# Kernel tuning notes

Measured on AMD Instinct MI355X. Metric: run time of the kernel, lower is better.

The kernel has to match this reference:

```python
import jax, jax.numpy as jnp
import numpy as np

B, S, D = 2, 2048, 1024
H, DK = 16, 64            # n_heads, d_k = d_model // n_heads
EXP = 4                   # pattern-separation expand_factor
ED = DK * EXP             # expanded_dim = 256
TOPK = 32                 # top-k kept after ReLU expansion
ALPHA = 0.05
TNT = 1.0                 # trace_norm_target


def setup_inputs() -> dict:
    key = jax.random.key(0)
    ks = jax.random.split(key, 8)
    sc = 1.0 / np.sqrt(D)
    x = jax.random.normal(ks[0], (B, S, D), jnp.float32)
    W_q = jax.random.normal(ks[1], (D, D), jnp.float32) * sc
    W_k = jax.random.normal(ks[2], (D, D), jnp.float32) * sc
    W_v = jax.random.normal(ks[3], (D, D), jnp.float32) * sc
    W_o = jax.random.normal(ks[4], (D, D), jnp.float32) * sc
    # trace buffers (non-zero so the trace read path actually matters)
    traces = jax.random.normal(ks[5], (H, DK, DK), jnp.float32) * 0.02
    value_traces = jax.random.normal(ks[6], (H, ED, DK), jnp.float32) * 0.02
    # frozen random expansion projection (dentate gyrus), W / sqrt(d_k)
    W_expand = jax.random.normal(ks[7], (DK, ED), jnp.float32) / np.sqrt(DK)
    return dict(x=x, W_q=W_q, W_k=W_k, W_v=W_v, W_o=W_o,
                traces=traces, value_traces=value_traces, W_expand=W_expand)


def _eff_alpha(T):
    # alpha / (1 + ||T_h||_F / trace_norm_target), shape (1, H, 1, 1)
    norms = jnp.sqrt(jnp.sum(T * T, axis=(1, 2)))
    return (ALPHA / (1.0 + norms / TNT)).reshape(1, -1, 1, 1)


def _forward(x, W_q, W_k, W_v, W_o, traces, value_traces, W_expand):
    b, s, d = x.shape
    def proj(W):
        return jnp.einsum('bsd,de->bse', x, W).reshape(b, s, H, DK).transpose(0, 2, 1, 3)
    Q, K, V = proj(W_q), proj(W_k), proj(W_v)  # (B, H, S, DK)

    scores = jnp.einsum('bhqd,bhkd->bhqk', Q, K)
    # score trace bias: alpha_eff * (Q @ T @ K^T)
    QT = jnp.einsum('bhqd,hde->bhqe', Q, traces)
    trace_scores = jnp.einsum('bhqe,bhke->bhqk', QT, K)
    scores = (scores + _eff_alpha(traces) * trace_scores) / np.sqrt(DK)
    A = jax.nn.softmax(scores, axis=-1)
    out = jnp.einsum('bhqk,bhkd->bhqd', A, V)

    # value trace read with use_key_q shift: address with previous token's Q
    Q_addr = jnp.concatenate([jnp.zeros_like(Q[:, :, :1, :]), Q[:, :, :-1, :]], axis=2)
    # pattern separation: frozen random expansion + ReLU + top-k sparsify
    Q_exp = jax.nn.relu(jnp.einsum('bhsd,de->bhse', Q_addr, W_expand))  # (B,H,S,ED)
    kth = jax.lax.top_k(Q_exp, TOPK)[0][..., -1:]
    Q_sparse = jnp.where(Q_exp >= kth, Q_exp, 0.0)  # == scatter of top-k vals (ties at 0 contribute 0)
    stored = jnp.einsum('bhse,hed->bhsd', Q_sparse, value_traces)
    out = out + _eff_alpha(value_traces) * stored

    out = out.transpose(0, 2, 1, 3).reshape(b, s, d)
    return jnp.einsum('bsd,de->bse', out, W_o)


def reference(x, W_q, W_k, W_v, W_o, traces, value_traces, W_expand):
    return _forward(x, W_q, W_k, W_v, W_o, traces, value_traces, W_expand)
```

## Files before the change

kernel.cpp:

```cpp
#include <hip/hip_runtime.h>
#include <stdint.h>

#define Bn 2
#define Sn 2048
#define Dn 1024
#define Hn 16
#define DKn 64
#define EDn 256

typedef __attribute__((ext_vector_type(8))) short bvec8;
typedef __attribute__((ext_vector_type(4))) float fvec4;

#define MFMA(a, b, c) __builtin_amdgcn_mfma_f32_16x16x32_bf16(a, b, c, 0, 0, 0)

__device__ __forceinline__ float b2f(unsigned short u) {
  return __uint_as_float(((unsigned)u) << 16);
}
__device__ __forceinline__ unsigned short f2b(float x) {
  unsigned u = __float_as_uint(x);
  u += 0x7fffu + ((u >> 16) & 1u);
  return (unsigned short)(u >> 16);
}
__device__ __forceinline__ void g2l(const unsigned short* g, unsigned short* l) {
  __builtin_amdgcn_global_load_lds(
      (const __attribute__((address_space(1))) void*)g,
      (__attribute__((address_space(3))) void*)l, 16, 0, 0);
}
__device__ __forceinline__ int dpp_sum16(int x) {
  x += __builtin_amdgcn_update_dpp(0, x, 0x140, 0xf, 0xf, true);
  x += __builtin_amdgcn_update_dpp(0, x, 0x141, 0xf, 0xf, true);
  x += __builtin_amdgcn_update_dpp(0, x, 0x1B, 0xf, 0xf, true);
  x += __builtin_amdgcn_update_dpp(0, x, 0xB1, 0xf, 0xf, true);
  return x;
}
__device__ __forceinline__ unsigned dpp_umax16(unsigned x) {
  unsigned t;
  t = (unsigned)__builtin_amdgcn_update_dpp(0, (int)x, 0x140, 0xf, 0xf, true);
  x = x > t ? x : t;
  t = (unsigned)__builtin_amdgcn_update_dpp(0, (int)x, 0x141, 0xf, 0xf, true);
  x = x > t ? x : t;
  t = (unsigned)__builtin_amdgcn_update_dpp(0, (int)x, 0x1B, 0xf, 0xf, true);
  x = x > t ? x : t;
  t = (unsigned)__builtin_amdgcn_update_dpp(0, (int)x, 0xB1, 0xf, 0xf, true);
  x = x > t ? x : t;
  return x;
}

__global__ __launch_bounds__(256) void k_alphas(
    const float* __restrict__ traces, const float* __restrict__ vtr,
    float* __restrict__ alphas) {
  int blk = blockIdx.x;
  const float* base;
  int n;
  if (blk < 16) { base = traces + blk * DKn * DKn; n = DKn * DKn; }
  else          { base = vtr + (blk - 16) * EDn * DKn; n = EDn * DKn; }
  float s = 0.f;
  for (int i = threadIdx.x; i < n; i += 256) { float v = base[i]; s += v * v; }
  __shared__ float red[256];
  red[threadIdx.x] = s;
  __syncthreads();
  for (int off = 128; off > 0; off >>= 1) {
    if (threadIdx.x < off) red[threadIdx.x] += red[threadIdx.x + off];
    __syncthreads();
  }
  if (threadIdx.x == 0) alphas[blk] = 0.05f / (1.f + sqrtf(red[0]));
}

__global__ __launch_bounds__(256) void k_trW(
    const float* __restrict__ w0, const float* __restrict__ w1,
    const float* __restrict__ w2, const float* __restrict__ w3,
    unsigned short* __restrict__ dst) {
  int z = blockIdx.z;
  const float* src = (z == 0) ? w0 : ((z == 1) ? w1 : ((z == 2) ? w2 : w3));
  unsigned short* d = dst + (size_t)z * Dn * Dn;
  __shared__ unsigned short Tl[64][72];
  int tid = threadIdx.x;
  int k0 = blockIdx.y * 64, n0 = blockIdx.x * 64;
#pragma unroll
  for (int i = 0; i < 4; ++i) {
    int q = tid + 256 * i;
    int kr = q >> 4, c4 = q & 15;
    float4 v = *(const float4*)&src[(size_t)(k0 + kr) * Dn + n0 + 4 * c4];
    ushort4 u;
    u.x = f2b(v.x); u.y = f2b(v.y); u.z = f2b(v.z); u.w = f2b(v.w);
    *(ushort4*)&Tl[kr][4 * c4] = u;
  }
  __syncthreads();
#pragma unroll
  for (int i = 0; i < 4; ++i) {
    int q = tid + 256 * i;
    int nr = q >> 4, c4 = q & 15;
    ushort4 u;
    u.x = Tl[4 * c4 + 0][nr]; u.y = Tl[4 * c4 + 1][nr];
    u.z = Tl[4 * c4 + 2][nr]; u.w = Tl[4 * c4 + 3][nr];
    *(ushort4*)&d[(size_t)(n0 + nr) * Dn + k0 + 4 * c4] = u;
  }
}

__global__ __launch_bounds__(256) void k_mkM(const float* __restrict__ tr,
                                             const float* __restrict__ alph,
                                             unsigned short* __restrict__ Mt) {
  int h = blockIdx.x;
  float a = alph[h] * 0.125f;
  const float* th = tr + (size_t)h * DKn * DKn;
  unsigned short* mh = Mt + (size_t)h * DKn * DKn;
  for (int i = threadIdx.x; i < DKn * DKn; i += 256) {
    int e = i >> 6, k = i & 63;
    float v = a * th[(size_t)k * DKn + e] + ((e == k) ? 0.125f : 0.f);
    mh[i] = f2b(v);
  }
}

__global__ __launch_bounds__(256) void k_trVT2(const float* __restrict__ vtr,
                                               const float* __restrict__ Wexp,
                                               unsigned short* __restrict__ VTt,
                                               unsigned short* __restrict__ WexpT) {
  int e0 = blockIdx.x * 64;
  int h = blockIdx.y;
  __shared__ unsigned short Tl[64][72];
  int tid = threadIdx.x;
  if (h < 16) {
    const float* src = vtr + (size_t)h * EDn * DKn;
    unsigned short* dst = VTt + (size_t)h * DKn * EDn;
#pragma unroll
    for (int i = 0; i < 4; ++i) {
      int q = tid + 256 * i;
      int er = q >> 4, c4 = q & 15;
      float4 v = *(const float4*)&src[(size_t)(e0 + er) * DKn + 4 * c4];
      ushort4 u;
      u.x = f2b(v.x); u.y = f2b(v.y); u.z = f2b(v.z); u.w = f2b(v.w);
      *(ushort4*)&Tl[er][4 * c4] = u;
    }
    __syncthreads();
#pragma unroll
    for (int i = 0; i < 4; ++i) {
      int q = tid + 256 * i;
      int dr = q >> 4, c4 = q & 15;
      ushort4 u;
      u.x = Tl[4 * c4 + 0][dr]; u.y = Tl[4 * c4 + 1][dr];
      u.z = Tl[4 * c4 + 2][dr]; u.w = Tl[4 * c4 + 3][dr];
      *(ushort4*)&dst[(size_t)dr * EDn + e0 + 4 * c4] = u;
    }
  } else {
#pragma unroll
    for (int i = 0; i < 4; ++i) {
      int q = tid + 256 * i;
      int dr = q >> 4, c4 = q & 15;
      float4 v = *(const float4*)&Wexp[(size_t)dr * EDn + e0 + 4 * c4];
      ushort4 u;
      u.x = f2b(v.x); u.y = f2b(v.y); u.z = f2b(v.z); u.w = f2b(v.w);
      *(ushort4*)&Tl[dr][4 * c4] = u;
    }
    __syncthreads();
#pragma unroll
    for (int i = 0; i < 4; ++i) {
      int q = tid + 256 * i;
      int er = q >> 4, c4 = q & 15;
      ushort4 u;
      u.x = Tl[4 * c4 + 0][er]; u.y = Tl[4 * c4 + 1][er];
      u.z = Tl[4 * c4 + 2][er]; u.w = Tl[4 * c4 + 3][er];
      *(ushort4*)&WexpT[(size_t)(e0 + er) * DKn + 4 * c4] = u;
    }
  }
}

__global__ __launch_bounds__(256) void k_xb(const float* __restrict__ x,
                                            unsigned short* __restrict__ xb) {
  size_t i = ((size_t)blockIdx.x * 256 + threadIdx.x) * 4;
  float4 v = *(const float4*)&x[i];
  ushort4 u;
  u.x = f2b(v.x); u.y = f2b(v.y); u.z = f2b(v.z); u.w = f2b(v.w);
  *(ushort4*)&xb[i] = u;
}

template <int MODE>
__global__ __launch_bounds__(256) void k_gemm(
    const unsigned short* __restrict__ Ab, const float* __restrict__ Af,
    const unsigned short* __restrict__ BtBase, unsigned short* __restrict__ Qb,
    unsigned short* __restrict__ Kb, unsigned short* __restrict__ VtOut,
    float* __restrict__ Cout) {
  const int z = (MODE == 0) ? blockIdx.z : 0;
  const unsigned short* Bt = BtBase + (size_t)z * Dn * Dn;
  __shared__ unsigned short As[128 * 32];
  __shared__ unsigned short Bs[128 * 32];
  const int tid = threadIdx.x;
  const int w = tid >> 6, lane = tid & 63, qd = lane >> 4, cc = lane & 15;
  const int m0 = blockIdx.y * 128, n0 = blockIdx.x * 128;
  const int mW = 64 * (w >> 1), nW = 64 * (w & 1);
  const int srow = lane >> 2;
  const int schk = 8 * ((lane & 3) ^ (srow & 3));
  const int r0 = 32 * w + srow, r1 = r0 + 16;
  fvec4 acc[4][4];
#pragma unroll
  for (int i = 0; i < 4; ++i)
#pragma unroll
    for (int j = 0; j < 4; ++j) acc[i][j] = (fvec4){0.f, 0.f, 0.f, 0.f};

  for (int k0 = 0; k0 < Dn; k0 += 32) {
    if (MODE == 0) {
      g2l(&Ab[(size_t)(m0 + r0) * Dn + k0 + schk], &As[1024 * w]);
      g2l(&Ab[(size_t)(m0 + r1) * Dn + k0 + schk], &As[1024 * w + 512]);
    } else {
#pragma unroll
      for (int i = 0; i < 4; ++i) {
        int q = tid + 256 * i;
        int row = q >> 3, c4 = q & 7;
        float4 v = *(const float4*)&Af[(size_t)(m0 + row) * Dn + k0 + 4 * c4];
        ushort4 u;
        u.x = f2b(v.x); u.y = f2b(v.y); u.z = f2b(v.z); u.w = f2b(v.w);
        *(ushort4*)&As[row * 32 + 8 * ((c4 >> 1) ^ (row & 3)) + 4 * (c4 & 1)] =
            u;
      }
    }
    g2l(&Bt[(size_t)(n0 + r0) * Dn + k0 + schk], &Bs[1024 * w]);
    g2l(&Bt[(size_t)(n0 + r1) * Dn + k0 + schk], &Bs[1024 * w + 512]);
    __syncthreads();
    bvec8 af[4], bf[4];
#pragma unroll
    for (int i = 0; i < 4; ++i) {
      int ra = mW + 16 * i + cc;
      af[i] = *(const bvec8*)&As[ra * 32 + 8 * (qd ^ (ra & 3))];
      int rb = nW + 16 * i + cc;
      bf[i] = *(const bvec8*)&Bs[rb * 32 + 8 * (qd ^ (rb & 3))];
    }
#pragma unroll
    for (int i = 0; i < 4; ++i)
#pragma unroll
      for (int j = 0; j < 4; ++j) acc[i][j] = MFMA(af[i], bf[j], acc[i][j]);
    __syncthreads();
  }
#pragma unroll
  for (int i = 0; i < 4; ++i)
#pragma unroll
    for (int j = 0; j < 4; ++j) {
      int rowb = m0 + mW + 16 * i + 4 * qd;
      int col = n0 + nW + 16 * j + cc;
      if (MODE == 0) {
        int b = rowb >> 11, s = rowb & 2047;
        int h = col >> 6, dk = col & 63;
        if (z == 2) {
          ushort4 u;
          u.x = f2b(acc[i][j][0]); u.y = f2b(acc[i][j][1]);
          u.z = f2b(acc[i][j][2]); u.w = f2b(acc[i][j][3]);
          *(ushort4*)&VtOut[(((size_t)(b * Hn + h)) * DKn + dk) * Sn + s] = u;
        } else {
          unsigned short* Cb = (z == 0) ? Qb : Kb;
#pragma unroll
          for (int r = 0; r < 4; ++r)
            Cb[(((size_t)(b * Hn + h)) * Sn + s + r) * DKn + dk] =
                f2b(acc[i][j][r]);
        }
      } else {
#pragma unroll
        for (int r = 0; r < 4; ++r)
          Cout[(size_t)(rowb + r) * Dn + col] = acc[i][j][r];
      }
    }
}

__global__ __launch_bounds__(256, 4) void k_pattsep(
    const unsigned short* __restrict__ Qb,
    const unsigned short* __restrict__ WexpT,
    const unsigned short* __restrict__ VTt,
    const float* __restrict__ alphas, float* __restrict__ AT) {
  __shared__ uint4 Ps4[4][256];
  const int tile = blockIdx.x, bh = blockIdx.y;
  const int b = bh >> 4, h = bh & 15;
  const int tid = threadIdx.x;
  const int w = tid >> 6, lane = tid & 63, qd = lane >> 4, cc = lane & 15;
  const float avt = alphas[16 + h];

  const unsigned short* vtab = VTt + (size_t)h * DKn * EDn;
  unsigned short* Pw = (unsigned short*)Ps4[w];

  const int s0 = tile * 64 + w * 16;
  bvec8 aq0 = {}, aq1 = {};
  const int srow = s0 + cc;
  if (srow > 0) {
    const unsigned short* qp = Qb + ((size_t)bh * Sn + srow - 1) * DKn;
    aq0 = *(const bvec8*)&qp[8 * qd];
    aq1 = *(const bvec8*)&qp[32 + 8 * qd];
  }
  fvec4 E[16];
#pragma unroll
  for (int j = 0; j < 16; ++j) {
    const int e = 16 * j + cc;
    const unsigned short* wr = WexpT + (size_t)e * 64;
    bvec8 b0 = *(const bvec8*)&wr[8 * qd];
    bvec8 b1 = *(const bvec8*)&wr[32 + 8 * qd];
    fvec4 zv = {0.f, 0.f, 0.f, 0.f};
    zv = MFMA(aq0, b0, zv);
    E[j] = MFMA(aq1, b1, zv);
  }
#pragma unroll
  for (int j = 0; j < 16; ++j)
#pragma unroll
    for (int r = 0; r < 4; ++r) E[j][r] = fmaxf(E[j][r], 0.f);

  float thr[4];
#pragma unroll
  for (int r = 0; r < 4; ++r) {
    unsigned mx = 0u;
#pragma unroll
    for (int j = 0; j < 16; ++j) {
      unsigned e = __float_as_uint(E[j][r]);
      mx = mx > e ? mx : e;
    }
    mx = dpp_umax16(mx);
    {
      unsigned o = (unsigned)__shfl_xor((int)mx, 16);
      mx = mx > o ? mx : o;
      o = (unsigned)__shfl_xor((int)mx, 32);
      mx = mx > o ? mx : o;
    }
    int bstart = (mx == 0u) ? -1 : (31 - __clz((int)mx));
    bstart = __builtin_amdgcn_readfirstlane(bstart);
    unsigned cur = 0u;
    bool done = false;
    for (int bit = bstart; bit >= 0; --bit) {
      unsigned cand = cur | (1u << bit);
      float t = __uint_as_float(cand);
      int cnt = 0;
#pragma unroll
      for (int j = 0; j < 16; ++j) cnt += (E[j][r] >= t) ? 1 : 0;
      cnt = dpp_sum16(cnt);
      if (!done && cnt >= 32) {
        cur = cand;
        if (cnt == 32) done = true;
      }
      if (__all(done)) break;
    }
    thr[r] = __uint_as_float(cur);
  }

  fvec4 acc2[4];
#pragma unroll
  for (int j2 = 0; j2 < 4; ++j2) acc2[j2] = (fvec4){0.f, 0.f, 0.f, 0.f};

#pragma unroll
  for (int half = 0; half < 2; ++half) {
#pragma unroll
    for (int j = 0; j < 8; ++j) {
      const int jj = j + 8 * half;
#pragma unroll
      for (int r = 0; r < 4; ++r) {
        float v = E[jj][r];
        bool sel = (v >= thr[r]) && (v > 0.f);
        int row = 4 * qd + r;
        int s = 16 * j + cc;
        int ch = (s >> 3) ^ (row & 7);
        Pw[row * 128 + ch * 8 + (s & 7)] = sel ? f2b(v) : (unsigned short)0;
      }
    }
#pragma unroll
    for (int j2 = 0; j2 < 4; ++j2) {
      const int d = 16 * j2 + cc;
      const unsigned short* vr = vtab + (size_t)d * 256;
#pragma unroll
      for (int c = 0; c < 4; ++c) {
        int cg = 4 * (c + 4 * half) + qd;
        bvec8 bv = *(const bvec8*)&vr[8 * cg];
        int ca = 4 * c + qd;
        bvec8 ap = *(const bvec8*)&Pw[cc * 128 + 8 * (ca ^ (cc & 7))];
        acc2[j2] = MFMA(ap, bv, acc2[j2]);
      }
    }
  }
#pragma unroll
  for (int j2 = 0; j2 < 4; ++j2)
#pragma unroll
    for (int r = 0; r < 4; ++r) {
      int row = s0 + 4 * qd + r;
      AT[((size_t)(b * Sn + row)) * Dn + h * DKn + 16 * j2 + cc] =
          avt * acc2[j2][r];
    }
}

__global__ __launch_bounds__(256, 2) void k_attn(
    const unsigned short* __restrict__ Qb, const unsigned short* __restrict__ Kb,
    const unsigned short* __restrict__ Vt, const unsigned short* __restrict__ Mt,
    float* __restrict__ AT) {
  __shared__ unsigned short Kd[3][64 * 64];
  __shared__ unsigned short Vl[3][64 * 64];
  __shared__ unsigned short Ps[4][32 * 64];
  const int bh = blockIdx.x, qt = blockIdx.y;
  const int b = bh >> 4, h = bh & 15;
  const int tid = threadIdx.x;
  const int w = tid >> 6, lane = tid & 63, qd = lane >> 4, cc = lane & 15;
  const float L2E = 1.4426950408889634f;
  const float NB = 23.083120654223414f;

  const unsigned short* qg = Qb + ((size_t)bh * Sn + qt * 128 + w * 32) * DKn;
  const unsigned short* mh = Mt + (size_t)h * DKn * DKn;
  unsigned short* Pw = Ps[w];
  bvec8 mb0[4], mb1[4];
#pragma unroll
  for (int j = 0; j < 4; ++j) {
    mb0[j] = *(const bvec8*)&mh[(size_t)(16 * j + cc) * DKn + 8 * qd];
    mb1[j] = *(const bvec8*)&mh[(size_t)(16 * j + cc) * DKn + 32 + 8 * qd];
  }
#pragma unroll
  for (int f = 0; f < 2; ++f) {
    bvec8 a0 = *(const bvec8*)&qg[(16 * f + cc) * DKn + 8 * qd];
    bvec8 a1 = *(const bvec8*)&qg[(16 * f + cc) * DKn + 32 + 8 * qd];
#pragma unroll
    for (int j = 0; j < 4; ++j) {
      fvec4 zz = {0.f, 0.f, 0.f, 0.f};
      zz = MFMA(a0, mb0[j], zz);
      zz = MFMA(a1, mb1[j], zz);
#pragma unroll
      for (int r = 0; r < 4; ++r) {
        int qr = 16 * f + 4 * qd + r;
        Pw[qr * 64 + 8 * ((2 * j + (cc >> 3)) ^ (qr & 7)) + (cc & 7)] =
            f2b(zz[r]);
      }
    }
  }
  bvec8 aqA0 = *(const bvec8*)&Pw[cc * 64 + 8 * (qd ^ (cc & 7))];
  bvec8 aqA1 = *(const bvec8*)&Pw[cc * 64 + 8 * ((qd + 4) ^ (cc & 7))];
  bvec8 aqB0 = *(const bvec8*)&Pw[(16 + cc) * 64 + 8 * (qd ^ (cc & 7))];
  bvec8 aqB1 = *(const bvec8*)&Pw[(16 + cc) * 64 + 8 * ((qd + 4) ^ (cc & 7))];

  float lsA = 0.f, lsB = 0.f;
  fvec4 OA[4], OB[4];
#pragma unroll
  for (int j = 0; j < 4; ++j) {
    OA[j] = (fvec4){0.f, 0.f, 0.f, 0.f};
    OB[j] = (fvec4){0.f, 0.f, 0.f, 0.f};
  }

  const int vrow = lane >> 3;
  const int vchk = 8 * ((lane & 7) ^ (vrow & 7));
  const unsigned short* kgb = Kb + (size_t)bh * Sn * DKn;
  const unsigned short* vgb = Vt + (size_t)bh * DKn * Sn;

  __builtin_amdgcn_sched_barrier(0);
#pragma unroll
  for (int p = 0; p < 2; ++p) {
    const unsigned short* kg = kgb + (size_t)p * 64 * DKn;
    g2l(&kg[(size_t)(16 * w + vrow) * 64 + vchk], &Kd[p][1024 * w]);
    g2l(&kg[(size_t)(16 * w + 8 + vrow) * 64 + vchk], &Kd[p][1024 * w + 512]);
    g2l(&vgb[(size_t)(16 * w + vrow) * Sn + p * 64 + vchk], &Vl[p][1024 * w]);
    g2l(&vgb[(size_t)(16 * w + 8 + vrow) * Sn + p * 64 + vchk],
        &Vl[p][1024 * w + 512]);
  }

  const int NT = Sn / 64;
  int buf = 0;
  for (int kt = 0; kt < NT; ++kt) {
    asm volatile("s_waitcnt vmcnt(4)" ::: "memory");
    __builtin_amdgcn_s_barrier();
    if (kt + 2 < NT) {
      int nb = buf + 2;
      if (nb >= 3) nb -= 3;
      const unsigned short* kg = kgb + (size_t)(kt + 2) * 64 * DKn;
      unsigned short* Kn = Kd[nb];
      unsigned short* Vn = Vl[nb];
      g2l(&kg[(size_t)(16 * w + vrow) * 64 + vchk], &Kn[1024 * w]);
      g2l(&kg[(size_t)(16 * w + 8 + vrow) * 64 + vchk], &Kn[1024 * w + 512]);
      g2l(&vgb[(size_t)(16 * w + vrow) * Sn + (kt + 2) * 64 + vchk],
          &Vn[1024 * w]);
      g2l(&vgb[(size_t)(16 * w + 8 + vrow) * Sn + (kt + 2) * 64 + vchk],
          &Vn[1024 * w + 512]);
    }
    __builtin_amdgcn_sched_barrier(0);
    const unsigned short* Kc = Kd[buf];
    const unsigned short* Vc = Vl[buf];
    fvec4 sA[4], sB[4];
#pragma unroll
    for (int j = 0; j < 4; ++j) {
      int rk = 16 * j + cc;
      bvec8 b0 = *(const bvec8*)&Kc[rk * 64 + 8 * (qd ^ (cc & 7))];
      bvec8 b1 = *(const bvec8*)&Kc[rk * 64 + 8 * ((qd + 4) ^ (cc & 7))];
      fvec4 z0 = {0.f, 0.f, 0.f, 0.f};
      z0 = MFMA(b0, aqA0, z0);
      sA[j] = MFMA(b1, aqA1, z0);
      fvec4 z1 = {0.f, 0.f, 0.f, 0.f};
      z1 = MFMA(b0, aqB0, z1);
      sB[j] = MFMA(b1, aqB1, z1);
    }
#pragma unroll
    for (int j = 0; j < 4; ++j) {
      float p0 = __builtin_amdgcn_exp2f(fmaf(sA[j][0], L2E, -NB));
      float p1 = __builtin_amdgcn_exp2f(fmaf(sA[j][1], L2E, -NB));
      float p2 = __builtin_amdgcn_exp2f(fmaf(sA[j][2], L2E, -NB));
      float p3 = __builtin_amdgcn_exp2f(fmaf(sA[j][3], L2E, -NB));
      lsA += (p0 + p1) + (p2 + p3);
      unsigned q01, q23;
      asm("v_cvt_pk_bf16_f32 %0, %1, %2" : "=v"(q01) : "v"(p0), "v"(p1));
      asm("v_cvt_pk_bf16_f32 %0, %1, %2" : "=v"(q23) : "v"(p2), "v"(p3));
      uint2 uu;
      uu.x = q01; uu.y = q23;
      *(uint2*)&Pw[cc * 64 + 4 * ((4 * j + qd) ^ cc)] = uu;
    }
#pragma unroll
    for (int j = 0; j < 4; ++j) {
      float p0 = __builtin_amdgcn_exp2f(fmaf(sB[j][0], L2E, -NB));
      float p1 = __builtin_amdgcn_exp2f(fmaf(sB[j][1], L2E, -NB));
      float p2 = __builtin_amdgcn_exp2f(fmaf(sB[j][2], L2E, -NB));
      float p3 = __builtin_amdgcn_exp2f(fmaf(sB[j][3], L2E, -NB));
      lsB += (p0 + p1) + (p2 + p3);
      unsigned q01, q23;
      asm("v_cvt_pk_bf16_f32 %0, %1, %2" : "=v"(q01) : "v"(p0), "v"(p1));
      asm("v_cvt_pk_bf16_f32 %0, %1, %2" : "=v"(q23) : "v"(p2), "v"(p3));
      uint2 uu;
      uu.x = q01; uu.y = q23;
      *(uint2*)&Pw[(16 + cc) * 64 + 4 * ((4 * j + qd) ^ cc)] = uu;
    }
    union U16 { bvec8 v; uint2 u[2]; } UA0, UA1, UB0, UB1;
    UA0.u[0] = *(const uint2*)&Pw[cc * 64 + 4 * ((2 * qd) ^ cc)];
    UA0.u[1] = *(const uint2*)&Pw[cc * 64 + 4 * ((2 * qd + 1) ^ cc)];
    UA1.u[0] = *(const uint2*)&Pw[cc * 64 + 4 * ((8 + 2 * qd) ^ cc)];
    UA1.u[1] = *(const uint2*)&Pw[cc * 64 + 4 * ((9 + 2 * qd) ^ cc)];
    UB0.u[0] = *(const uint2*)&Pw[(16 + cc) * 64 + 4 * ((2 * qd) ^ cc)];
    UB0.u[1] = *(const uint2*)&Pw[(16 + cc) * 64 + 4 * ((2 * qd + 1) ^ cc)];
    UB1.u[0] = *(const uint2*)&Pw[(16 + cc) * 64 + 4 * ((8 + 2 * qd) ^ cc)];
    UB1.u[1] = *(const uint2*)&Pw[(16 + cc) * 64 + 4 * ((9 + 2 * qd) ^ cc)];
#pragma unroll
    for (int j = 0; j < 4; ++j) {
      int rv = 16 * j + cc;
      bvec8 v0 = *(const bvec8*)&Vc[rv * 64 + 8 * (qd ^ (cc & 7))];
      bvec8 v1 = *(const bvec8*)&Vc[rv * 64 + 8 * ((qd + 4) ^ (cc & 7))];
      OA[j] = MFMA(UA0.v, v0, OA[j]);
      OA[j] = MFMA(UA1.v, v1, OA[j]);
      OB[j] = MFMA(UB0.v, v0, OB[j]);
      OB[j] = MFMA(UB1.v, v1, OB[j]);
    }
    buf = (buf == 2) ? 0 : buf + 1;
  }
  lsA += __shfl_xor(lsA, 16);
  lsA += __shfl_xor(lsA, 32);
  lsB += __shfl_xor(lsB, 16);
  lsB += __shfl_xor(lsB, 32);
  float liA = 1.f / lsA, liB = 1.f / lsB;
  float iA[4], iB[4];
#pragma unroll
  for (int r = 0; r < 4; ++r) {
    iA[r] = __shfl(liA, 4 * qd + r);
    iB[r] = __shfl(liB, 4 * qd + r);
  }
#pragma unroll
  for (int j = 0; j < 4; ++j)
#pragma unroll
    for (int r = 0; r < 4; ++r) {
      int rowA = qt * 128 + w * 32 + 4 * qd + r;
      float* pA = AT + ((size_t)(b * Sn + rowA)) * Dn + h * DKn + 16 * j + cc;
      *pA += OA[j][r] * iA[r];
      float* pB = pA + 16 * (size_t)Dn;
      *pB += OB[j][r] * iB[r];
    }
}

extern "C" void kernel_launch(void* const* d_in, const int* in_sizes, int n_in,
                              void* d_out, int out_size, void* d_ws,
                              size_t ws_size, hipStream_t stream) {
  const float* x = (const float*)d_in[0];
  const float* Wq = (const float*)d_in[1];
  const float* Wk = (const float*)d_in[2];
  const float* Wv = (const float*)d_in[3];
  const float* Wo = (const float*)d_in[4];
  const float* traces = (const float*)d_in[5];
  const float* vtr = (const float*)d_in[6];
  const float* Wexp = (const float*)d_in[7];

  const size_t NQ = (size_t)Bn * Hn * Sn * DKn;
  unsigned short* Qb = (unsigned short*)d_ws;
  unsigned short* Kb = Qb + NQ;
  unsigned short* Vt = Kb + NQ;
  unsigned short* Wt = Vt + NQ;
  unsigned short* Mt = Wt + NQ;
  unsigned short* WexpT = Mt + 65536;
  unsigned short* VTt = WexpT + 16384;
  float* alph = (float*)(VTt + 262144);
  float* AT = alph + 32;
  unsigned short* xb = (unsigned short*)AT;

  k_alphas<<<32, 256, 0, stream>>>(traces, vtr, alph);
  k_trW<<<dim3(16, 16, 4), 256, 0, stream>>>(Wq, Wk, Wv, Wo, Wt);
  k_mkM<<<16, 256, 0, stream>>>(traces, alph, Mt);
  k_trVT2<<<dim3(4, 17), 256, 0, stream>>>(vtr, Wexp, VTt, WexpT);
  k_xb<<<4096, 256, 0, stream>>>(x, xb);
  k_gemm<0><<<dim3(8, 32, 3), 256, 0, stream>>>(xb, nullptr, Wt, Qb, Kb, Vt,
                                                nullptr);
  k_pattsep<<<dim3(32, 32), 256, 0, stream>>>(Qb, WexpT, VTt, alph, AT);
  k_attn<<<dim3(32, 16), 256, 0, stream>>>(Qb, Kb, Vt, Mt, AT);
  k_gemm<1><<<dim3(8, 32, 1), 256, 0, stream>>>(
      nullptr, AT, Wt + 3 * (size_t)Dn * Dn, nullptr, nullptr, nullptr,
      (float*)d_out);
}
```

Measured before the change: 277.5 us.

## Fuse prep kernels, reorder attention before pattern-sep, add MFMA priority hints

Merges the x-to-bf16 conversion into the weight-transpose launch as an extra z-slice, and computes the score-trace alpha inside k_mkM so k_alphas only handles value traces. These changes remove kernel launches. Attention now runs before pattern separation, so attention writes AT directly and pattern-sep accumulates into it, which swaps which kernel does the read-modify-write. s_setprio is raised around the MFMA blocks in the attention loop to favour matrix issue across waves.

```diff
diff --git a/kernel.cpp b/kernel.cpp
--- a/kernel.cpp
+++ b/kernel.cpp
@@ -47,13 +47,10 @@
 }
 
 __global__ __launch_bounds__(256) void k_alphas(
-    const float* __restrict__ traces, const float* __restrict__ vtr,
-    float* __restrict__ alphas) {
+    const float* __restrict__ vtr, float* __restrict__ alphas) {
   int blk = blockIdx.x;
-  const float* base;
-  int n;
-  if (blk < 16) { base = traces + blk * DKn * DKn; n = DKn * DKn; }
-  else          { base = vtr + (blk - 16) * EDn * DKn; n = EDn * DKn; }
+  const float* base = vtr + (size_t)blk * EDn * DKn;
+  int n = EDn * DKn;
   float s = 0.f;
   for (int i = threadIdx.x; i < n; i += 256) { float v = base[i]; s += v * v; }
   __shared__ float red[256];
@@ -63,18 +60,33 @@
     if (threadIdx.x < off) red[threadIdx.x] += red[threadIdx.x + off];
     __syncthreads();
   }
-  if (threadIdx.x == 0) alphas[blk] = 0.05f / (1.f + sqrtf(red[0]));
+  if (threadIdx.x == 0) alphas[16 + blk] = 0.05f / (1.f + sqrtf(red[0]));
 }
 
 __global__ __launch_bounds__(256) void k_trW(
     const float* __restrict__ w0, const float* __restrict__ w1,
     const float* __restrict__ w2, const float* __restrict__ w3,
-    unsigned short* __restrict__ dst) {
+    const float* __restrict__ x, unsigned short* __restrict__ dst,
+    unsigned short* __restrict__ xb) {
   int z = blockIdx.z;
+  int tid = threadIdx.x;
+  if (z == 4) {
+    int rbase = blockIdx.y * 256, c0 = blockIdx.x * 64;
+#pragma unroll
+    for (int i = 0; i < 16; ++i) {
+      int q = tid + 256 * i;
+      int rr = q >> 4, c4 = q & 15;
+      size_t idx = (size_t)(rbase + rr) * Dn + c0 + 4 * c4;
+      float4 v = *(const float4*)&x[idx];
+      ushort4 u;
+      u.x = f2b(v.x); u.y = f2b(v.y); u.z = f2b(v.z); u.w = f2b(v.w);
+      *(ushort4*)&xb[idx] = u;
+    }
+    return;
+  }
   const float* src = (z == 0) ? w0 : ((z == 1) ? w1 : ((z == 2) ? w2 : w3));
   unsigned short* d = dst + (size_t)z * Dn * Dn;
   __shared__ unsigned short Tl[64][72];
-  int tid = threadIdx.x;
   int k0 = blockIdx.y * 64, n0 = blockIdx.x * 64;
 #pragma unroll
   for (int i = 0; i < 4; ++i) {
@@ -98,11 +110,25 @@
 }
 
 __global__ __launch_bounds__(256) void k_mkM(const float* __restrict__ tr,
-                                             const float* __restrict__ alph,
                                              unsigned short* __restrict__ Mt) {
   int h = blockIdx.x;
-  float a = alph[h] * 0.125f;
   const float* th = tr + (size_t)h * DKn * DKn;
+  float s = 0.f;
+  for (int i = threadIdx.x; i < DKn * DKn; i += 256) {
+    float v = th[i];
+    s += v * v;
+  }
+  __shared__ float red[256];
+  red[threadIdx.x] = s;
+  __syncthreads();
+  for (int off = 128; off > 0; off >>= 1) {
+    if (threadIdx.x < off) red[threadIdx.x] += red[threadIdx.x + off];
+    __syncthreads();
+  }
+  __shared__ float a_s;
+  if (threadIdx.x == 0) a_s = 0.125f * 0.05f / (1.f + sqrtf(red[0]));
+  __syncthreads();
+  float a = a_s;
   unsigned short* mh = Mt + (size_t)h * DKn * DKn;
   for (int i = threadIdx.x; i < DKn * DKn; i += 256) {
     int e = i >> 6, k = i & 63;
@@ -162,15 +188,6 @@
       *(ushort4*)&WexpT[(size_t)(e0 + er) * DKn + 4 * c4] = u;
     }
   }
-}
-
-__global__ __launch_bounds__(256) void k_xb(const float* __restrict__ x,
-                                            unsigned short* __restrict__ xb) {
-  size_t i = ((size_t)blockIdx.x * 256 + threadIdx.x) * 4;
-  float4 v = *(const float4*)&x[i];
-  ushort4 u;
-  u.x = f2b(v.x); u.y = f2b(v.y); u.z = f2b(v.z); u.w = f2b(v.w);
-  *(ushort4*)&xb[i] = u;
 }
 
 template <int MODE>
@@ -371,8 +388,8 @@
 #pragma unroll
     for (int r = 0; r < 4; ++r) {
       int row = s0 + 4 * qd + r;
-      AT[((size_t)(b * Sn + row)) * Dn + h * DKn + 16 * j2 + cc] =
-          avt * acc2[j2][r];
+      float* p = AT + ((size_t)(b * Sn + row)) * Dn + h * DKn + 16 * j2 + cc;
+      *p += avt * acc2[j2][r];
     }
 }
 
@@ -467,6 +484,7 @@
     const unsigned short* Kc = Kd[buf];
     const unsigned short* Vc = Vl[buf];
     fvec4 sA[4], sB[4];
+    __builtin_amdgcn_s_setprio(1);
 #pragma unroll
     for (int j = 0; j < 4; ++j) {
       int rk = 16 * j + cc;
@@ -479,6 +497,7 @@
       z1 = MFMA(b0, aqB0, z1);
       sB[j] = MFMA(b1, aqB1, z1);
     }
+    __builtin_amdgcn_s_setprio(0);
 #pragma unroll
     for (int j = 0; j < 4; ++j) {
       float p0 = __builtin_amdgcn_exp2f(fmaf(sA[j][0], L2E, -NB));
@@ -516,6 +535,7 @@
     UB0.u[1] = *(const uint2*)&Pw[(16 + cc) * 64 + 4 * ((2 * qd + 1) ^ cc)];
     UB1.u[0] = *(const uint2*)&Pw[(16 + cc) * 64 + 4 * ((8 + 2 * qd) ^ cc)];
     UB1.u[1] = *(const uint2*)&Pw[(16 + cc) * 64 + 4 * ((9 + 2 * qd) ^ cc)];
+    __builtin_amdgcn_s_setprio(1);
 #pragma unroll
     for (int j = 0; j < 4; ++j) {
       int rv = 16 * j + cc;
@@ -526,6 +546,7 @@
       OB[j] = MFMA(UB0.v, v0, OB[j]);
       OB[j] = MFMA(UB1.v, v1, OB[j]);
     }
+    __builtin_amdgcn_s_setprio(0);
     buf = (buf == 2) ? 0 : buf + 1;
   }
   lsA += __shfl_xor(lsA, 16);
@@ -545,9 +566,9 @@
     for (int r = 0; r < 4; ++r) {
       int rowA = qt * 128 + w * 32 + 4 * qd + r;
       float* pA = AT + ((size_t)(b * Sn + rowA)) * Dn + h * DKn + 16 * j + cc;
-      *pA += OA[j][r] * iA[r];
+      *pA = OA[j][r] * iA[r];
       float* pB = pA + 16 * (size_t)Dn;
-      *pB += OB[j][r] * iB[r];
+      *pB = OB[j][r] * iB[r];
     }
 }
 
@@ -575,15 +596,14 @@
   float* AT = alph + 32;
   unsigned short* xb = (unsigned short*)AT;
 
-  k_alphas<<<32, 256, 0, stream>>>(traces, vtr, alph);
-  k_trW<<<dim3(16, 16, 4), 256, 0, stream>>>(Wq, Wk, Wv, Wo, Wt);
-  k_mkM<<<16, 256, 0, stream>>>(traces, alph, Mt);
+  k_alphas<<<16, 256, 0, stream>>>(vtr, alph);
+  k_trW<<<dim3(16, 16, 5), 256, 0, stream>>>(Wq, Wk, Wv, Wo, x, Wt, xb);
+  k_mkM<<<16, 256, 0, stream>>>(traces, Mt);
   k_trVT2<<<dim3(4, 17), 256, 0, stream>>>(vtr, Wexp, VTt, WexpT);
-  k_xb<<<4096, 256, 0, stream>>>(x, xb);
   k_gemm<0><<<dim3(8, 32, 3), 256, 0, stream>>>(xb, nullptr, Wt, Qb, Kb, Vt,
                                                 nullptr);
+  k_attn<<<dim3(32, 16), 256, 0, stream>>>(Qb, Kb, Vt, Mt, AT);
   k_pattsep<<<dim3(32, 32), 256, 0, stream>>>(Qb, WexpT, VTt, alph, AT);
-  k_attn<<<dim3(32, 16), 256, 0, stream>>>(Qb, Kb, Vt, Mt, AT);
   k_gemm<1><<<dim3(8, 32, 1), 256, 0, stream>>>(
       nullptr, AT, Wt + 3 * (size_t)Dn * Dn, nullptr, nullptr, nullptr,
       (float*)d_out);
```

After: 283.4 us. 2.1% more time.
